# Kernel optimization log

Measured on AMD Instinct MI355X. Metric: run time of the kernel, lower is better.

The kernel has to match this reference:

```python
import jax, jax.numpy as jnp
import numpy as np

D_MODEL = 1024
NUM_HEADS = 16
D_K = D_MODEL // NUM_HEADS
THETA = 10000.0


def _rope(x, pos):
    # x: [B, H, T, d_k], pos: [T]
    inv_freq = 1.0 / (THETA ** (jnp.arange(0, D_K, 2, dtype=jnp.float32) / D_K))  # [d_k/2]
    ang = pos.astype(jnp.float32)[:, None] * inv_freq[None, :]                    # [T, d_k/2]
    cos = jnp.repeat(jnp.cos(ang), 2, axis=-1)                                    # [T, d_k]
    sin = jnp.repeat(jnp.sin(ang), 2, axis=-1)
    x = x.astype(jnp.float32)
    x0 = x[..., ::2]
    x1 = x[..., 1::2]
    rot = jnp.stack((-x1, x0), axis=-1).reshape(x.shape)  # rotate_half, interleaved
    return x * cos + rot * sin


def setup_inputs() -> dict:
    key = jax.random.key(0)
    k1, k2, k3 = jax.random.split(key, 3)
    B, T = 2, 2048
    sigma_qkv = float(np.sqrt(2.0 / (D_MODEL + 3 * D_MODEL)))
    sigma_out = float(np.sqrt(2.0 / (D_MODEL + D_MODEL)))
    return {
        "x": jax.random.normal(k1, (B, T, D_MODEL), dtype=jnp.float32),
        "w_qkv": jax.random.normal(k2, (3 * D_MODEL, D_MODEL), dtype=jnp.float32) * sigma_qkv,
        "w_out": jax.random.normal(k3, (D_MODEL, D_MODEL), dtype=jnp.float32) * sigma_out,
    }


def reference(x, w_qkv, w_out):
    B, T, _ = x.shape
    qkv = jnp.einsum("btd,ed->bte", x, w_qkv)                 # [B, T, 3*D]
    q, k, v = jnp.split(qkv, 3, axis=-1)

    def split_head(t):
        return t.reshape(B, T, NUM_HEADS, D_K).transpose(0, 2, 1, 3)  # [B, H, T, d_k]

    q, k, v = split_head(q), split_head(k), split_head(v)
    pos = jnp.arange(T)
    q = _rope(q, pos)
    k = _rope(k, pos)

    scores = jnp.einsum("bhqd,bhkd->bhqk", q, k) / jnp.sqrt(jnp.float32(D_K))
    causal = jnp.tril(jnp.ones((T, T), dtype=bool))            # True = keep
    scores = jnp.where(causal[None, None], scores, -jnp.inf)
    attn = jax.nn.softmax(scores, axis=-1)
    out = jnp.einsum("bhqk,bhkd->bhqd", attn, v)               # [B, H, T, d_k]
    out = out.transpose(0, 2, 1, 3).reshape(B, T, D_MODEL)
    return jnp.einsum("btd,ed->bte", out, w_out)
```

## Files before the change

kernel.cpp:

```cpp
#include <hip/hip_runtime.h>
#include <cstdint>
#include <cstddef>

#define BB 2
#define TT 2048
#define DMODEL 1024
#define NHEADS 16
#define DK 64

typedef short short8 __attribute__((ext_vector_type(8)));
typedef unsigned short ushort8 __attribute__((ext_vector_type(8)));
typedef float floatx4 __attribute__((ext_vector_type(4)));
typedef _Float16 half4 __attribute__((ext_vector_type(4)));

#define MFMA_PV(A, B, C) __builtin_amdgcn_mfma_f32_16x16x16f16(A, B, C, 0, 0, 0)

__device__ __forceinline__ unsigned short f2bf(float f) {
    uint32_t u = __builtin_bit_cast(uint32_t, f);
    uint32_t r = (u + 0x7FFFu + ((u >> 16) & 1u)) >> 16;
    return (unsigned short)r;
}
__device__ __forceinline__ float bf2f(unsigned short s) {
    uint32_t u = ((uint32_t)s) << 16;
    return __builtin_bit_cast(float, u);
}

#define GLDS16(g, l) __builtin_amdgcn_global_load_lds( \
    (const __attribute__((address_space(1))) void*)(g), \
    (__attribute__((address_space(3))) void*)(l), 16, 0, 0)

__global__ void castk3(const float* __restrict__ x, unsigned short* __restrict__ xb,
                       const float* __restrict__ wq, unsigned short* __restrict__ wqb,
                       const float* __restrict__ wo, unsigned short* __restrict__ wob) {
    int bid = blockIdx.x;
    const float* in;
    unsigned short* out;
    int base;
    if (bid < 4096)       { in = x;  out = xb;  base = bid * 1024; }
    else if (bid < 7168)  { in = wq; out = wqb; base = (bid - 4096) * 1024; }
    else                  { in = wo; out = wob; base = (bid - 7168) * 1024; }
    int i = base + threadIdx.x * 4;
    float4 v = *(const float4*)(in + i);
    ushort4 o;
    o.x = f2bf(v.x); o.y = f2bf(v.y); o.z = f2bf(v.z); o.w = f2bf(v.w);
    *(ushort4*)(out + i) = o;
}

template <typename OUT>
__global__ __launch_bounds__(256)
void gemm_bt(const unsigned short* __restrict__ A, const unsigned short* __restrict__ B,
             OUT* __restrict__ C, int M, int N, int K) {
    __shared__ unsigned short As[128 * 32];
    __shared__ unsigned short Bs[128 * 32];

    const int tid  = threadIdx.x;
    const int lane = tid & 63;
    const int w    = tid >> 6;
    const int wm   = w & 1;
    const int wn   = w >> 1;
    const int quad = lane >> 4;
    const int l16  = lane & 15;

    const int m0 = blockIdx.y * 128;
    const int n0 = blockIdx.x * 128;

    floatx4 acc[4][4];
#pragma unroll
    for (int a = 0; a < 4; a++)
#pragma unroll
        for (int b = 0; b < 4; b++)
            acc[a][b] = (floatx4){0.f, 0.f, 0.f, 0.f};

    const int c0 = w * 128 + lane;
    const int c1 = c0 + 64;
    const int r0 = c0 >> 2, cc0 = (c0 & 3) ^ ((r0 >> 1) & 3);
    const int r1 = c1 >> 2, cc1 = (c1 & 3) ^ ((r1 >> 1) & 3);

    const unsigned short* gA0 = A + (size_t)(m0 + r0) * K + cc0 * 8;
    const unsigned short* gA1 = A + (size_t)(m0 + r1) * K + cc1 * 8;
    const unsigned short* gB0 = B + (size_t)(n0 + r0) * K + cc0 * 8;
    const unsigned short* gB1 = B + (size_t)(n0 + r1) * K + cc1 * 8;

    unsigned short* lA0 = &As[(2 * w + 0) * 512];
    unsigned short* lA1 = &As[(2 * w + 1) * 512];
    unsigned short* lB0 = &Bs[(2 * w + 0) * 512];
    unsigned short* lB1 = &Bs[(2 * w + 1) * 512];

    const int rsw = (l16 >> 1) & 3;

    for (int k0 = 0; k0 < K; k0 += 32) {
        __syncthreads();
        GLDS16(gA0 + k0, lA0);
        GLDS16(gA1 + k0, lA1);
        GLDS16(gB0 + k0, lB0);
        GLDS16(gB1 + k0, lB1);
        __syncthreads();

        short8 af[4], bf[4];
#pragma unroll
        for (int t = 0; t < 4; t++) {
            af[t] = *(const short8*)&As[(wm * 64 + t * 16 + l16) * 32 + (quad ^ rsw) * 8];
            bf[t] = *(const short8*)&Bs[(wn * 64 + t * 16 + l16) * 32 + (quad ^ rsw) * 8];
        }
#pragma unroll
        for (int tm = 0; tm < 4; tm++)
#pragma unroll
            for (int tn = 0; tn < 4; tn++)
                acc[tm][tn] = __builtin_amdgcn_mfma_f32_16x16x32_bf16(
                    af[tm], bf[tn], acc[tm][tn], 0, 0, 0);
    }

#pragma unroll
    for (int tm = 0; tm < 4; tm++) {
#pragma unroll
        for (int tn = 0; tn < 4; tn++) {
#pragma unroll
            for (int r = 0; r < 4; r++) {
                int m = m0 + wm * 64 + tm * 16 + quad * 4 + r;
                int n = n0 + wn * 64 + tn * 16 + l16;
                if constexpr (sizeof(OUT) == 4)
                    C[(size_t)m * N + n] = acc[tm][tn][r];
                else
                    C[(size_t)m * N + n] = f2bf(acc[tm][tn][r]);
            }
        }
    }
}

__global__ __launch_bounds__(256)
void ropevt(const unsigned short* __restrict__ qkv,
            unsigned short* __restrict__ qb, unsigned short* __restrict__ kb,
            unsigned short* __restrict__ vtb) {
    __shared__ unsigned short tile[64][72];
    const int tid = threadIdx.x;
    const int bh  = blockIdx.y;
    const int b = bh >> 4, h = bh & 15;
    const int t0 = blockIdx.x * 64;

    const float QS = 0.18033688f;
#pragma unroll
    for (int rep = 0; rep < 8; rep++) {
        int idx  = rep * 256 + tid;
        int p    = idx & 31;
        int trow = idx >> 5;
        int t    = t0 + trow;

        size_t src = (size_t)(b * TT + t) * 3072 + h * 64 + 2 * p;
        ushort2 qu = *(const ushort2*)(qkv + src);
        ushort2 ku = *(const ushort2*)(qkv + src + 1024);
        float qx = bf2f(qu.x), qy = bf2f(qu.y);
        float kx = bf2f(ku.x), ky = bf2f(ku.y);

        float invf = __powf(10000.f, -((float)(2 * p)) / 64.f);
        float ang  = (float)t * invf;
        float sn, cs;
        __sincosf(ang, &sn, &cs);

        size_t dst = ((size_t)bh * TT + t) * 64 + 2 * p;
        ushort2 qo, ko;
        qo.x = f2bf((qx * cs - qy * sn) * QS); qo.y = f2bf((qy * cs + qx * sn) * QS);
        ko.x = f2bf(kx * cs - ky * sn); ko.y = f2bf(ky * cs + kx * sn);
        *(ushort2*)(qb + dst) = qo;
        *(ushort2*)(kb + dst) = ko;
    }

    const int row = tid >> 2;
    const unsigned short* src = qkv + ((size_t)(b * TT) + t0 + row) * 3072 + 2048 + h * 64;
    {
        int cb = (tid & 3) * 16;
        ushort8 v0 = *(const ushort8*)(src + cb);
        ushort8 v1 = *(const ushort8*)(src + cb + 8);
#pragma unroll
        for (int i = 0; i < 8; i++) tile[row][cb + i] = v0[i];
#pragma unroll
        for (int i = 0; i < 8; i++) tile[row][cb + 8 + i] = v1[i];
    }
    __syncthreads();

    const int d  = tid >> 2;
    const int tc = tid & 3;
    const int hs = (d & 1) * 4;
    ushort8 o0, o1;
#pragma unroll
    for (int i = 0; i < 8; i++) {
        _Float16 hv = (_Float16)bf2f(tile[tc * 16 + (i ^ hs)][d]);
        o0[i] = __builtin_bit_cast(unsigned short, hv);
    }
#pragma unroll
    for (int i = 0; i < 8; i++) {
        _Float16 hv = (_Float16)bf2f(tile[tc * 16 + 8 + (i ^ hs)][d]);
        o1[i] = __builtin_bit_cast(unsigned short, hv);
    }
    unsigned short* dst = vtb + ((size_t)bh * 64 + d) * TT + t0 + tc * 16;
    *(ushort8*)(dst) = o0;
    *(ushort8*)(dst + 8) = o1;
}

__global__ __launch_bounds__(256, 5)
void attn_mfma(const unsigned short* __restrict__ qb,
               const unsigned short* __restrict__ kb,
               const unsigned short* __restrict__ vtb,
               unsigned short* __restrict__ out) {
    __shared__ unsigned short Ks[2][64 * 64];
    __shared__ unsigned short Vs[2][64 * 64];

    const int tid  = threadIdx.x;
    const int lane = tid & 63;
    const int w    = tid >> 6;
    const int quad = lane >> 4;
    const int l16  = lane & 15;

    const int bh    = blockIdx.x;
    const int qtile = gridDim.y - 1 - blockIdx.y;
    const int q0    = qtile * 64;

    const unsigned short* Qp = qb + ((size_t)bh * TT + q0 + w * 16) * 64;
    const unsigned short* Kp = kb + (size_t)bh * TT * 64;
    const unsigned short* Vp = vtb + (size_t)bh * 64 * TT;

    short8 aq[2];
#pragma unroll
    for (int ks = 0; ks < 2; ks++)
        aq[ks] = *(const short8*)(Qp + (size_t)l16 * 64 + ks * 32 + quad * 8);

    floatx4 Oacc[4];
#pragma unroll
    for (int dt = 0; dt < 4; dt++) Oacc[dt] = (floatx4){0.f, 0.f, 0.f, 0.f};
    float m = -1e30f, l = 0.f;

    const int ntiles = qtile + 1;

#define STAGE(IT, P)                                                                      \
    {                                                                                     \
        const int j0s = (IT) * 64;                                                        \
        _Pragma("unroll")                                                                 \
        for (int rep = 0; rep < 2; rep++) {                                               \
            int c    = rep * 256 + tid;                                                   \
            int row  = c >> 3, sl = c & 7;                                                \
            GLDS16(Kp + (size_t)(j0s + row) * 64 + (sl ^ (row & 7)) * 8, &Ks[P][c * 8]);  \
            GLDS16(Vp + (size_t)row * TT + j0s + (sl ^ ((row >> 1) & 7)) * 8,             \
                   &Vs[P][c * 8]);                                                        \
        }                                                                                 \
    }

    STAGE(0, 0);
    __syncthreads();

    const int ksw = l16 & 7;
    const int vsw = (l16 >> 1) & 7;
    const int vsub = ((quad & 1) ^ (l16 & 1)) * 4;

    for (int it = 0; it < ntiles; ++it) {
        const int p = it & 1;
        if (it + 1 < ntiles) STAGE(it + 1, p ^ 1);

        floatx4 sacc[4];
#pragma unroll
        for (int nt = 0; nt < 4; nt++) sacc[nt] = (floatx4){0.f, 0.f, 0.f, 0.f};
#pragma unroll
        for (int ks = 0; ks < 2; ks++)
#pragma unroll
            for (int nt = 0; nt < 4; nt++) {
                short8 kf = *(const short8*)&Ks[p][(nt * 16 + l16) * 64 + ((ks * 4 + quad) ^ ksw) * 8];
                sacc[nt] = __builtin_amdgcn_mfma_f32_16x16x32_bf16(kf, aq[ks], sacc[nt], 0, 0, 0);
            }

        if (it == qtile) {
            const int qg = w * 16 + l16;
#pragma unroll
            for (int nt = 0; nt < 4; nt++)
#pragma unroll
                for (int r = 0; r < 4; r++)
                    if (nt * 16 + quad * 4 + r > qg) sacc[nt][r] = -1e30f;
        }

        float mx = sacc[0][0];
#pragma unroll
        for (int nt = 0; nt < 4; nt++)
#pragma unroll
            for (int r = 0; r < 4; r++) mx = fmaxf(mx, sacc[nt][r]);
        mx = fmaxf(mx, __shfl_xor(mx, 16));
        mx = fmaxf(mx, __shfl_xor(mx, 32));
        float mnew  = fmaxf(m, mx);
        float alpha = __builtin_amdgcn_exp2f(m - mnew);
        m = mnew;
        float psum = 0.f;
#pragma unroll
        for (int nt = 0; nt < 4; nt++)
#pragma unroll
            for (int r = 0; r < 4; r++) {
                float pv = __builtin_amdgcn_exp2f(sacc[nt][r] - mnew);
                sacc[nt][r] = pv;
                psum += pv;
            }
        psum += __shfl_xor(psum, 16);
        psum += __shfl_xor(psum, 32);
        l = l * alpha + psum;

#pragma unroll
        for (int dt = 0; dt < 4; dt++)
#pragma unroll
            for (int r = 0; r < 4; r++) Oacc[dt][r] *= alpha;

        half4 bp[4];
#pragma unroll
        for (int nt = 0; nt < 4; nt++) {
            half4 h;
            h[0] = (_Float16)sacc[nt][0];
            h[1] = (_Float16)sacc[nt][1];
            h[2] = (_Float16)sacc[nt][2];
            h[3] = (_Float16)sacc[nt][3];
            bp[nt] = h;
        }

#pragma unroll
        for (int dt = 0; dt < 4; dt++)
#pragma unroll
            for (int nt = 0; nt < 4; nt++) {
                int c = nt * 2 + (quad >> 1);
                half4 vf = *(const half4*)&Vs[p][(dt * 16 + l16) * 64 + (c ^ vsw) * 8 + vsub];
                Oacc[dt] = MFMA_PV(vf, bp[nt], Oacc[dt]);
            }

        __syncthreads();
    }
#undef STAGE

    const int b = bh >> 4, h = bh & 15;
    const float inv = 1.f / l;
    const size_t base = ((size_t)(b * TT + q0 + w * 16 + l16)) * DMODEL + h * 64 + quad * 4;
#pragma unroll
    for (int dt = 0; dt < 4; dt++) {
        ushort4 pk;
        pk.x = f2bf(Oacc[dt][0] * inv);
        pk.y = f2bf(Oacc[dt][1] * inv);
        pk.z = f2bf(Oacc[dt][2] * inv);
        pk.w = f2bf(Oacc[dt][3] * inv);
        *(ushort4*)(out + base + dt * 16) = pk;
    }
}

extern "C" void kernel_launch(void* const* d_in, const int* in_sizes, int n_in,
                              void* d_out, int out_size, void* d_ws, size_t ws_size,
                              hipStream_t stream) {
    const float* x     = (const float*)d_in[0];
    const float* w_qkv = (const float*)d_in[1];
    const float* w_out = (const float*)d_in[2];
    float* out = (float*)d_out;

    char* ws = (char*)d_ws;

    unsigned short* xb   = (unsigned short*)(ws);
    unsigned short* wqb  = (unsigned short*)(ws + 8388608);
    unsigned short* wob  = (unsigned short*)(ws + 14680064);
    unsigned short* qkvb = (unsigned short*)(ws + 16777216);
    unsigned short* qb   = (unsigned short*)(ws + 41943040);
    unsigned short* kb   = (unsigned short*)(ws + 50331648);
    unsigned short* vtb  = (unsigned short*)(ws + 58720256);
    unsigned short* attb = (unsigned short*)(ws + 67108864);

    castk3<<<8192, 256, 0, stream>>>(x, xb, w_qkv, wqb, w_out, wob);

    gemm_bt<unsigned short><<<dim3(3072 / 128, 4096 / 128), 256, 0, stream>>>(
        xb, wqb, qkvb, 4096, 3072, 1024);

    ropevt<<<dim3(TT / 64, BB * NHEADS), 256, 0, stream>>>(qkvb, qb, kb, vtb);

    attn_mfma<<<dim3(BB * NHEADS, TT / 64), 256, 0, stream>>>(qb, kb, vtb, attb);

    gemm_bt<float><<<dim3(1024 / 128, 4096 / 128), 256, 0, stream>>>(
        attb, wob, out, 4096, 1024, 1024);
}
```

Baseline: 191.7 us.

## Process 128-query tiles per block with two 16-row groups per wave

```diff
diff --git a/kernel.cpp b/kernel.cpp
--- a/kernel.cpp
+++ b/kernel.cpp
@@ -196,7 +196,7 @@
     *(ushort8*)(dst + 8) = o1;
 }
 
-__global__ __launch_bounds__(256, 5)
+__global__ __launch_bounds__(256, 3)
 void attn_mfma(const unsigned short* __restrict__ qb,
                const unsigned short* __restrict__ kb,
                const unsigned short* __restrict__ vtb,
@@ -210,25 +210,32 @@
     const int quad = lane >> 4;
     const int l16  = lane & 15;
 
-    const int bh    = blockIdx.x;
-    const int qtile = gridDim.y - 1 - blockIdx.y;
-    const int q0    = qtile * 64;
-
-    const unsigned short* Qp = qb + ((size_t)bh * TT + q0 + w * 16) * 64;
+    const int bh = blockIdx.x;
+    const int y   = blockIdx.y;
+    const int qb2 = (y & 1) ? (y >> 1) : (15 - (y >> 1));
+    const int Q0  = qb2 * 128;
+
+    const unsigned short* Qp = qb + ((size_t)bh * TT + Q0 + w * 32) * 64;
     const unsigned short* Kp = kb + (size_t)bh * TT * 64;
     const unsigned short* Vp = vtb + (size_t)bh * 64 * TT;
 
-    short8 aq[2];
-#pragma unroll
-    for (int ks = 0; ks < 2; ks++)
-        aq[ks] = *(const short8*)(Qp + (size_t)l16 * 64 + ks * 32 + quad * 8);
-
-    floatx4 Oacc[4];
-#pragma unroll
-    for (int dt = 0; dt < 4; dt++) Oacc[dt] = (floatx4){0.f, 0.f, 0.f, 0.f};
-    float m = -1e30f, l = 0.f;
-
-    const int ntiles = qtile + 1;
+    short8 aq[2][2];
+#pragma unroll
+    for (int g = 0; g < 2; g++)
+#pragma unroll
+        for (int ks = 0; ks < 2; ks++)
+            aq[g][ks] = *(const short8*)(Qp + (size_t)(g * 16 + l16) * 64 + ks * 32 + quad * 8);
+
+    floatx4 Oacc[2][4];
+#pragma unroll
+    for (int g = 0; g < 2; g++)
+#pragma unroll
+        for (int dt = 0; dt < 4; dt++) Oacc[g][dt] = (floatx4){0.f, 0.f, 0.f, 0.f};
+    float m[2] = {-1e30f, -1e30f}, l[2] = {0.f, 0.f};
+
+    const int ntiles = 2 * qb2 + 2;
+    const int myDiag = 2 * qb2 + (w >> 1);
+    const int qloc0  = (w & 1) * 32 + l16;
 
 #define STAGE(IT, P)                                                                      \
     {                                                                                     \
@@ -254,89 +261,108 @@
         const int p = it & 1;
         if (it + 1 < ntiles) STAGE(it + 1, p ^ 1);
 
-        floatx4 sacc[4];
-#pragma unroll
-        for (int nt = 0; nt < 4; nt++) sacc[nt] = (floatx4){0.f, 0.f, 0.f, 0.f};
-#pragma unroll
-        for (int ks = 0; ks < 2; ks++)
-#pragma unroll
-            for (int nt = 0; nt < 4; nt++) {
-                short8 kf = *(const short8*)&Ks[p][(nt * 16 + l16) * 64 + ((ks * 4 + quad) ^ ksw) * 8];
-                sacc[nt] = __builtin_amdgcn_mfma_f32_16x16x32_bf16(kf, aq[ks], sacc[nt], 0, 0, 0);
+        if (it <= myDiag) {
+            short8 kf[2][4];
+#pragma unroll
+            for (int ks = 0; ks < 2; ks++)
+#pragma unroll
+                for (int nt = 0; nt < 4; nt++)
+                    kf[ks][nt] = *(const short8*)&Ks[p][(nt * 16 + l16) * 64 + ((ks * 4 + quad) ^ ksw) * 8];
+            half4 vf[4][4];
+#pragma unroll
+            for (int dt = 0; dt < 4; dt++)
+#pragma unroll
+                for (int nt = 0; nt < 4; nt++) {
+                    int c = nt * 2 + (quad >> 1);
+                    vf[dt][nt] = *(const half4*)&Vs[p][(dt * 16 + l16) * 64 + (c ^ vsw) * 8 + vsub];
+                }
+
+#pragma unroll
+            for (int g = 0; g < 2; g++) {
+                floatx4 sacc[4];
+#pragma unroll
+                for (int nt = 0; nt < 4; nt++) sacc[nt] = (floatx4){0.f, 0.f, 0.f, 0.f};
+#pragma unroll
+                for (int ks = 0; ks < 2; ks++)
+#pragma unroll
+                    for (int nt = 0; nt < 4; nt++)
+                        sacc[nt] = __builtin_amdgcn_mfma_f32_16x16x32_bf16(
+                            kf[ks][nt], aq[g][ks], sacc[nt], 0, 0, 0);
+
+                if (it == myDiag) {
+                    const int qg = qloc0 + g * 16;
+#pragma unroll
+                    for (int nt = 0; nt < 4; nt++)
+#pragma unroll
+                        for (int r = 0; r < 4; r++)
+                            if (nt * 16 + quad * 4 + r > qg) sacc[nt][r] = -1e30f;
+                }
+
+                float mx = sacc[0][0];
+#pragma unroll
+                for (int nt = 0; nt < 4; nt++)
+#pragma unroll
+                    for (int r = 0; r < 4; r++) mx = fmaxf(mx, sacc[nt][r]);
+                mx = fmaxf(mx, __shfl_xor(mx, 16));
+                mx = fmaxf(mx, __shfl_xor(mx, 32));
+                float mnew  = fmaxf(m[g], mx);
+                float alpha = __builtin_amdgcn_exp2f(m[g] - mnew);
+                m[g] = mnew;
+                float psum = 0.f;
+#pragma unroll
+                for (int nt = 0; nt < 4; nt++)
+#pragma unroll
+                    for (int r = 0; r < 4; r++) {
+                        float pv = __builtin_amdgcn_exp2f(sacc[nt][r] - mnew);
+                        sacc[nt][r] = pv;
+                        psum += pv;
+                    }
+                psum += __shfl_xor(psum, 16);
+                psum += __shfl_xor(psum, 32);
+                l[g] = l[g] * alpha + psum;
+
+#pragma unroll
+                for (int dt = 0; dt < 4; dt++)
+#pragma unroll
+                    for (int r = 0; r < 4; r++) Oacc[g][dt][r] *= alpha;
+
+                half4 bp[4];
+#pragma unroll
+                for (int nt = 0; nt < 4; nt++) {
+                    half4 h;
+                    h[0] = (_Float16)sacc[nt][0];
+                    h[1] = (_Float16)sacc[nt][1];
+                    h[2] = (_Float16)sacc[nt][2];
+                    h[3] = (_Float16)sacc[nt][3];
+                    bp[nt] = h;
+                }
+
+#pragma unroll
+                for (int dt = 0; dt < 4; dt++)
+#pragma unroll
+                    for (int nt = 0; nt < 4; nt++)
+                        Oacc[g][dt] = MFMA_PV(vf[dt][nt], bp[nt], Oacc[g][dt]);
             }
-
-        if (it == qtile) {
-            const int qg = w * 16 + l16;
-#pragma unroll
-            for (int nt = 0; nt < 4; nt++)
-#pragma unroll
-                for (int r = 0; r < 4; r++)
-                    if (nt * 16 + quad * 4 + r > qg) sacc[nt][r] = -1e30f;
         }
 
-        float mx = sacc[0][0];
-#pragma unroll
-        for (int nt = 0; nt < 4; nt++)
-#pragma unroll
-            for (int r = 0; r < 4; r++) mx = fmaxf(mx, sacc[nt][r]);
-        mx = fmaxf(mx, __shfl_xor(mx, 16));
-        mx = fmaxf(mx, __shfl_xor(mx, 32));
-        float mnew  = fmaxf(m, mx);
-        float alpha = __builtin_amdgcn_exp2f(m - mnew);
-        m = mnew;
-        float psum = 0.f;
-#pragma unroll
-        for (int nt = 0; nt < 4; nt++)
-#pragma unroll
-            for (int r = 0; r < 4; r++) {
-                float pv = __builtin_amdgcn_exp2f(sacc[nt][r] - mnew);
-                sacc[nt][r] = pv;
-                psum += pv;
-            }
-        psum += __shfl_xor(psum, 16);
-        psum += __shfl_xor(psum, 32);
-        l = l * alpha + psum;
-
-#pragma unroll
-        for (int dt = 0; dt < 4; dt++)
-#pragma unroll
-            for (int r = 0; r < 4; r++) Oacc[dt][r] *= alpha;
-
-        half4 bp[4];
-#pragma unroll
-        for (int nt = 0; nt < 4; nt++) {
-            half4 h;
-            h[0] = (_Float16)sacc[nt][0];
-            h[1] = (_Float16)sacc[nt][1];
-            h[2] = (_Float16)sacc[nt][2];
-            h[3] = (_Float16)sacc[nt][3];
-            bp[nt] = h;
+        __syncthreads();
+    }
+#undef STAGE
+
+    const int b = bh >> 4, h = bh & 15;
+#pragma unroll
+    for (int g = 0; g < 2; g++) {
+        const float inv = 1.f / l[g];
+        const size_t base = ((size_t)(b * TT + Q0 + w * 32 + g * 16 + l16)) * DMODEL + h * 64 + quad * 4;
+#pragma unroll
+        for (int dt = 0; dt < 4; dt++) {
+            ushort4 pk;
+            pk.x = f2bf(Oacc[g][dt][0] * inv);
+            pk.y = f2bf(Oacc[g][dt][1] * inv);
+            pk.z = f2bf(Oacc[g][dt][2] * inv);
+            pk.w = f2bf(Oacc[g][dt][3] * inv);
+            *(ushort4*)(out + base + dt * 16) = pk;
         }
-
-#pragma unroll
-        for (int dt = 0; dt < 4; dt++)
-#pragma unroll
-            for (int nt = 0; nt < 4; nt++) {
-                int c = nt * 2 + (quad >> 1);
-                half4 vf = *(const half4*)&Vs[p][(dt * 16 + l16) * 64 + (c ^ vsw) * 8 + vsub];
-                Oacc[dt] = MFMA_PV(vf, bp[nt], Oacc[dt]);
-            }
-
-        __syncthreads();
-    }
-#undef STAGE
-
-    const int b = bh >> 4, h = bh & 15;
-    const float inv = 1.f / l;
-    const size_t base = ((size_t)(b * TT + q0 + w * 16 + l16)) * DMODEL + h * 64 + quad * 4;
-#pragma unroll
-    for (int dt = 0; dt < 4; dt++) {
-        ushort4 pk;
-        pk.x = f2bf(Oacc[dt][0] * inv);
-        pk.y = f2bf(Oacc[dt][1] * inv);
-        pk.z = f2bf(Oacc[dt][2] * inv);
-        pk.w = f2bf(Oacc[dt][3] * inv);
-        *(ushort4*)(out + base + dt * 16) = pk;
     }
 }
 
@@ -366,7 +392,7 @@
 
     ropevt<<<dim3(TT / 64, BB * NHEADS), 256, 0, stream>>>(qkvb, qb, kb, vtb);
 
-    attn_mfma<<<dim3(BB * NHEADS, TT / 64), 256, 0, stream>>>(qb, kb, vtb, attb);
+    attn_mfma<<<dim3(BB * NHEADS, TT / 128), 256, 0, stream>>>(qb, kb, vtb, attb);
 
     gemm_bt<float><<<dim3(1024 / 128, 4096 / 128), 256, 0, stream>>>(
         attb, wob, out, 4096, 1024, 1024);
```

New measurement: 203.4 us. 1.06x slower.

## Fuse RoPE and V transpose into QKV GEMM epilogue

Applied to the files above, without the earlier changes.

```diff
diff --git a/kernel.cpp b/kernel.cpp
--- a/kernel.cpp
+++ b/kernel.cpp
@@ -46,10 +46,11 @@
     *(ushort4*)(out + i) = o;
 }
 
-template <typename OUT>
 __global__ __launch_bounds__(256)
-void gemm_bt(const unsigned short* __restrict__ A, const unsigned short* __restrict__ B,
-             OUT* __restrict__ C, int M, int N, int K) {
+void gemm_qkv(const unsigned short* __restrict__ A, const unsigned short* __restrict__ B,
+              unsigned short* __restrict__ qb, unsigned short* __restrict__ kb,
+              unsigned short* __restrict__ vtb) {
+    const int K = 1024;
     __shared__ unsigned short As[128 * 32];
     __shared__ unsigned short Bs[128 * 32];
 
@@ -110,6 +111,118 @@
                     af[tm], bf[tn], acc[tm][tn], 0, 0, 0);
     }
 
+    const int region = n0 >> 10;
+    if (region < 2) {
+        const float QS = 0.18033688f;
+        unsigned short* dstb = (region == 0) ? qb : kb;
+#pragma unroll
+        for (int tn = 0; tn < 4; tn++) {
+            const int n = n0 + wn * 64 + tn * 16 + l16;
+            const int f = n & 1023;
+            const int h = f >> 6;
+            const int d = f & 63;
+            const int p = d >> 1;
+            const float invf = __powf(10000.f, -((float)(2 * p)) / 64.f);
+            const bool odd = (d & 1) != 0;
+#pragma unroll
+            for (int tm = 0; tm < 4; tm++) {
+#pragma unroll
+                for (int r = 0; r < 4; r++) {
+                    int mIdx = m0 + wm * 64 + tm * 16 + quad * 4 + r;
+                    int bb = mIdx >> 11, t = mIdx & 2047;
+                    float val = acc[tm][tn][r];
+                    float part = __shfl_xor(val, 1);
+                    float sn, cs;
+                    __sincosf((float)t * invf, &sn, &cs);
+                    float o = odd ? (val * cs + part * sn) : (val * cs - part * sn);
+                    if (region == 0) o *= QS;
+                    dstb[((size_t)(bb * NHEADS + h) * TT + t) * 64 + d] = f2bf(o);
+                }
+            }
+        }
+    } else {
+#pragma unroll
+        for (int tn = 0; tn < 4; tn++) {
+            const int f = (n0 + wn * 64 + tn * 16 + l16) & 1023;
+            const int h = f >> 6;
+            const int d = f & 63;
+            const int hs = (d & 1) * 4;
+#pragma unroll
+            for (int tm = 0; tm < 4; tm++) {
+                int m0r = m0 + wm * 64 + tm * 16 + quad * 4;
+                int bb = m0r >> 11, t0r = m0r & 2047;
+                half4 hv;
+#pragma unroll
+                for (int r = 0; r < 4; r++) hv[r] = (_Float16)acc[tm][tn][r];
+                *(half4*)((_Float16*)vtb + ((size_t)(bb * NHEADS + h) * 64 + d) * TT + (t0r ^ hs)) = hv;
+            }
+        }
+    }
+}
+
+__global__ __launch_bounds__(256)
+void gemm_bt(const unsigned short* __restrict__ A, const unsigned short* __restrict__ B,
+             float* __restrict__ C, int M, int N, int K) {
+    __shared__ unsigned short As[128 * 32];
+    __shared__ unsigned short Bs[128 * 32];
+
+    const int tid  = threadIdx.x;
+    const int lane = tid & 63;
+    const int w    = tid >> 6;
+    const int wm   = w & 1;
+    const int wn   = w >> 1;
+    const int quad = lane >> 4;
+    const int l16  = lane & 15;
+
+    const int m0 = blockIdx.y * 128;
+    const int n0 = blockIdx.x * 128;
+
+    floatx4 acc[4][4];
+#pragma unroll
+    for (int a = 0; a < 4; a++)
+#pragma unroll
+        for (int b = 0; b < 4; b++)
+            acc[a][b] = (floatx4){0.f, 0.f, 0.f, 0.f};
+
+    const int c0 = w * 128 + lane;
+    const int c1 = c0 + 64;
+    const int r0 = c0 >> 2, cc0 = (c0 & 3) ^ ((r0 >> 1) & 3);
+    const int r1 = c1 >> 2, cc1 = (c1 & 3) ^ ((r1 >> 1) & 3);
+
+    const unsigned short* gA0 = A + (size_t)(m0 + r0) * K + cc0 * 8;
+    const unsigned short* gA1 = A + (size_t)(m0 + r1) * K + cc1 * 8;
+    const unsigned short* gB0 = B + (size_t)(n0 + r0) * K + cc0 * 8;
+    const unsigned short* gB1 = B + (size_t)(n0 + r1) * K + cc1 * 8;
+
+    unsigned short* lA0 = &As[(2 * w + 0) * 512];
+    unsigned short* lA1 = &As[(2 * w + 1) * 512];
+    unsigned short* lB0 = &Bs[(2 * w + 0) * 512];
+    unsigned short* lB1 = &Bs[(2 * w + 1) * 512];
+
+    const int rsw = (l16 >> 1) & 3;
+
+    for (int k0 = 0; k0 < K; k0 += 32) {
+        __syncthreads();
+        GLDS16(gA0 + k0, lA0);
+        GLDS16(gA1 + k0, lA1);
+        GLDS16(gB0 + k0, lB0);
+        GLDS16(gB1 + k0, lB1);
+        __syncthreads();
+
+        short8 af[4], bf[4];
+#pragma unroll
+        for (int t = 0; t < 4; t++) {
+            af[t] = *(const short8*)&As[(wm * 64 + t * 16 + l16) * 32 + (quad ^ rsw) * 8];
+            bf[t] = *(const short8*)&Bs[(wn * 64 + t * 16 + l16) * 32 + (quad ^ rsw) * 8];
+        }
+#pragma unroll
+        for (int tm = 0; tm < 4; tm++)
+#pragma unroll
+            for (int tn = 0; tn < 4; tn++)
+                acc[tm][tn] = __builtin_amdgcn_mfma_f32_16x16x32_bf16(
+                    af[tm], bf[tn], acc[tm][tn], 0, 0, 0);
+    }
+
 #pragma unroll
     for (int tm = 0; tm < 4; tm++) {
 #pragma unroll
@@ -118,82 +231,10 @@
             for (int r = 0; r < 4; r++) {
                 int m = m0 + wm * 64 + tm * 16 + quad * 4 + r;
                 int n = n0 + wn * 64 + tn * 16 + l16;
-                if constexpr (sizeof(OUT) == 4)
-                    C[(size_t)m * N + n] = acc[tm][tn][r];
-                else
-                    C[(size_t)m * N + n] = f2bf(acc[tm][tn][r]);
-            }
-        }
-    }
-}
-
-__global__ __launch_bounds__(256)
-void ropevt(const unsigned short* __restrict__ qkv,
-            unsigned short* __restrict__ qb, unsigned short* __restrict__ kb,
-            unsigned short* __restrict__ vtb) {
-    __shared__ unsigned short tile[64][72];
-    const int tid = threadIdx.x;
-    const int bh  = blockIdx.y;
-    const int b = bh >> 4, h = bh & 15;
-    const int t0 = blockIdx.x * 64;
-
-    const float QS = 0.18033688f;
-#pragma unroll
-    for (int rep = 0; rep < 8; rep++) {
-        int idx  = rep * 256 + tid;
-        int p    = idx & 31;
-        int trow = idx >> 5;
-        int t    = t0 + trow;
-
-        size_t src = (size_t)(b * TT + t) * 3072 + h * 64 + 2 * p;
-        ushort2 qu = *(const ushort2*)(qkv + src);
-        ushort2 ku = *(const ushort2*)(qkv + src + 1024);
-        float qx = bf2f(qu.x), qy = bf2f(qu.y);
-        float kx = bf2f(ku.x), ky = bf2f(ku.y);
-
-        float invf = __powf(10000.f, -((float)(2 * p)) / 64.f);
-        float ang  = (float)t * invf;
-        float sn, cs;
-        __sincosf(ang, &sn, &cs);
-
-        size_t dst = ((size_t)bh * TT + t) * 64 + 2 * p;
-        ushort2 qo, ko;
-        qo.x = f2bf((qx * cs - qy * sn) * QS); qo.y = f2bf((qy * cs + qx * sn) * QS);
-        ko.x = f2bf(kx * cs - ky * sn); ko.y = f2bf(ky * cs + kx * sn);
-        *(ushort2*)(qb + dst) = qo;
-        *(ushort2*)(kb + dst) = ko;
-    }
-
-    const int row = tid >> 2;
-    const unsigned short* src = qkv + ((size_t)(b * TT) + t0 + row) * 3072 + 2048 + h * 64;
-    {
-        int cb = (tid & 3) * 16;
-        ushort8 v0 = *(const ushort8*)(src + cb);
-        ushort8 v1 = *(const ushort8*)(src + cb + 8);
-#pragma unroll
-        for (int i = 0; i < 8; i++) tile[row][cb + i] = v0[i];
-#pragma unroll
-        for (int i = 0; i < 8; i++) tile[row][cb + 8 + i] = v1[i];
-    }
-    __syncthreads();
-
-    const int d  = tid >> 2;
-    const int tc = tid & 3;
-    const int hs = (d & 1) * 4;
-    ushort8 o0, o1;
-#pragma unroll
-    for (int i = 0; i < 8; i++) {
-        _Float16 hv = (_Float16)bf2f(tile[tc * 16 + (i ^ hs)][d]);
-        o0[i] = __builtin_bit_cast(unsigned short, hv);
-    }
-#pragma unroll
-    for (int i = 0; i < 8; i++) {
-        _Float16 hv = (_Float16)bf2f(tile[tc * 16 + 8 + (i ^ hs)][d]);
-        o1[i] = __builtin_bit_cast(unsigned short, hv);
-    }
-    unsigned short* dst = vtb + ((size_t)bh * 64 + d) * TT + t0 + tc * 16;
-    *(ushort8*)(dst) = o0;
-    *(ushort8*)(dst + 8) = o1;
+                C[(size_t)m * N + n] = acc[tm][tn][r];
+            }
+        }
+    }
 }
 
 __global__ __launch_bounds__(256, 5)
@@ -353,21 +394,16 @@
     unsigned short* xb   = (unsigned short*)(ws);
     unsigned short* wqb  = (unsigned short*)(ws + 8388608);
     unsigned short* wob  = (unsigned short*)(ws + 14680064);
-    unsigned short* qkvb = (unsigned short*)(ws + 16777216);
-    unsigned short* qb   = (unsigned short*)(ws + 41943040);
-    unsigned short* kb   = (unsigned short*)(ws + 50331648);
-    unsigned short* vtb  = (unsigned short*)(ws + 58720256);
-    unsigned short* attb = (unsigned short*)(ws + 67108864);
+    unsigned short* qb   = (unsigned short*)(ws + 16777216);
+    unsigned short* kb   = (unsigned short*)(ws + 25165824);
+    unsigned short* vtb  = (unsigned short*)(ws + 33554432);
+    unsigned short* attb = (unsigned short*)(ws + 41943040);
 
     castk3<<<8192, 256, 0, stream>>>(x, xb, w_qkv, wqb, w_out, wob);
 
-    gemm_bt<unsigned short><<<dim3(3072 / 128, 4096 / 128), 256, 0, stream>>>(
-        xb, wqb, qkvb, 4096, 3072, 1024);
-
-    ropevt<<<dim3(TT / 64, BB * NHEADS), 256, 0, stream>>>(qkvb, qb, kb, vtb);
+    gemm_qkv<<<dim3(3072 / 128, 4096 / 128), 256, 0, stream>>>(xb, wqb, qb, kb, vtb);
 
     attn_mfma<<<dim3(BB * NHEADS, TT / 64), 256, 0, stream>>>(qb, kb, vtb, attb);
 
-    gemm_bt<float><<<dim3(1024 / 128, 4096 / 128), 256, 0, stream>>>(
-        attb, wob, out, 4096, 1024, 1024);
-}
+    gemm_bt<<<dim3(1024 / 128, 4096 / 128), 256, 0, stream>>>(attb, wob, out, 4096, 1024, 1024);
+}
```

New measurement: 209.5 us. +9.3%, slower.
